# Kernel optimization log

Measured on AMD Instinct MI355X. Metric: run time of the kernel, lower is better.

## Reference

```python
import jax, jax.numpy as jnp
import numpy as np

NUM_HEADS = 12


def setup_inputs() -> dict:
    key = jax.random.key(0)
    k1, k2, k3 = jax.random.split(key, 3)
    B, N, C = 64, 320, 768
    x = jax.random.normal(k1, (B, N, C), dtype=jnp.float32)
    W_qkv = jax.random.normal(k2, (C, 3 * C), dtype=jnp.float32) * (C ** -0.5)
    W_proj = jax.random.normal(k3, (C, C), dtype=jnp.float32) * (C ** -0.5)
    b_proj = jnp.zeros((C,), dtype=jnp.float32)
    return {"x": x, "W_qkv": W_qkv, "W_proj": W_proj, "b_proj": b_proj,
            "t_h": 8, "t_w": 8, "s_h": 16, "s_w": 16}


def reference(x, W_qkv, W_proj, b_proj, t_h, t_w, s_h, s_w):
    B, N, C = x.shape
    H = NUM_HEADS
    Dh = C // H
    scale = Dh ** -0.5
    L = t_h * t_w  # template length; search length = s_h*s_w = N - L

    qkv = (x @ W_qkv).reshape(B, N, 3, H, Dh)
    q = jnp.transpose(qkv[:, :, 0], (0, 2, 1, 3))  # [B,H,N,Dh]
    k = jnp.transpose(qkv[:, :, 1], (0, 2, 1, 3))
    v = jnp.transpose(qkv[:, :, 2], (0, 2, 1, 3))

    q_mt, q_s = q[:, :, :L], q[:, :, L:]
    k_mt = k[:, :, :L]
    v_mt = v[:, :, :L]

    # Template self-attention (template attends only to template)
    attn_mt = jax.nn.softmax(jnp.einsum('bhqd,bhkd->bhqk', q_mt * scale, k_mt), axis=-1)
    x_mt = jnp.einsum('bhqk,bhkd->bhqd', attn_mt, v_mt)  # [B,H,L,Dh]

    # Search cross-attention (search attends to all tokens)
    attn_s = jax.nn.softmax(jnp.einsum('bhqd,bhkd->bhqk', q_s * scale, k), axis=-1)
    x_s = jnp.einsum('bhqk,bhkd->bhqd', attn_s, v)  # [B,H,N-L,Dh]

    x_mt = jnp.transpose(x_mt, (0, 2, 1, 3)).reshape(B, L, C)
    x_s = jnp.transpose(x_s, (0, 2, 1, 3)).reshape(B, N - L, C)
    out = jnp.concatenate([x_mt, x_s], axis=1)  # [B,N,C]
    out = out @ W_proj + b_proj
    return out
```

## Files before the change

### kernel.cpp

```cpp
#include <hip/hip_runtime.h>
#include <hip/hip_bf16.h>
#include <stdint.h>

#define BB 64
#define NN 320
#define CC 768
#define HH 12
#define DH 64
#define NC3 2304
#define MROWS (BB*NN)

typedef __attribute__((ext_vector_type(8))) short short8;
typedef __attribute__((ext_vector_type(4))) float f32x4;
typedef __attribute__((ext_vector_type(8))) __bf16 bf16x8;

union BF8U { short8 s; bf16x8 b; };
static __device__ __forceinline__ bf16x8 asbf(short8 v){ BF8U u; u.s = v; return u.b; }

#define MFMA16(a,b,c) __builtin_amdgcn_mfma_f32_16x16x32_bf16((a),(b),(c),0,0,0)

static __device__ __forceinline__ void gload16(const void* g, void* l){
  __builtin_amdgcn_global_load_lds(
      (const __attribute__((address_space(1))) void*)g,
      (__attribute__((address_space(3))) void*)l, 16, 0, 0);
}

__global__ __launch_bounds__(256) void convert_wT(
    const float* __restrict__ in, __hip_bfloat16* __restrict__ outT,
    int K, int Nc)
{
  __shared__ __hip_bfloat16 t[64][72];
  const int n0 = blockIdx.x * 64, k0 = blockIdx.y * 64;
  const int tid = threadIdx.x;
  const int tx = tid & 15, ty = tid >> 4;

  #pragma unroll
  for (int i = 0; i < 4; ++i){
    int kl = ty + i * 16;
    float4 v = *reinterpret_cast<const float4*>(&in[(size_t)(k0 + kl) * Nc + n0 + tx * 4]);
    t[tx*4+0][kl] = __float2bfloat16(v.x);
    t[tx*4+1][kl] = __float2bfloat16(v.y);
    t[tx*4+2][kl] = __float2bfloat16(v.z);
    t[tx*4+3][kl] = __float2bfloat16(v.w);
  }
  __syncthreads();
  #pragma unroll
  for (int j = 0; j < 2; ++j){
    int nl = (tid >> 3) + j * 32;
    int kl = (tid & 7) * 8;
    short8 v = *reinterpret_cast<const short8*>(&t[nl][kl]);
    *reinterpret_cast<short8*>(&outT[(size_t)(n0 + nl) * K + k0 + kl]) = v;
  }
}

__global__ __launch_bounds__(256) void convert_x(
    const float* __restrict__ X, __hip_bfloat16* __restrict__ Xb)
{
  size_t i = ((size_t)blockIdx.x * 256 + threadIdx.x) * 8;
  float4 a = *reinterpret_cast<const float4*>(&X[i]);
  float4 b = *reinterpret_cast<const float4*>(&X[i + 4]);
  __hip_bfloat16 t[8] = {__float2bfloat16(a.x), __float2bfloat16(a.y),
                         __float2bfloat16(a.z), __float2bfloat16(a.w),
                         __float2bfloat16(b.x), __float2bfloat16(b.y),
                         __float2bfloat16(b.z), __float2bfloat16(b.w)};
  *reinterpret_cast<short8*>(&Xb[i]) = *reinterpret_cast<const short8*>(t);
}

#define BM 128
#define BN 128
#define BK 64
#define NT (CC/BK)

__global__ __launch_bounds__(256, 4) void gemm_qkv(
    const __hip_bfloat16* __restrict__ Xb,
    const __hip_bfloat16* __restrict__ WT,
    __hip_bfloat16* __restrict__ qb,
    __hip_bfloat16* __restrict__ kb,
    __hip_bfloat16* __restrict__ vt)
{
  __shared__ __hip_bfloat16 As[BM][BK];
  __shared__ __hip_bfloat16 Bs[BN][BK];
  const int tid = threadIdx.x;
  const int bm = blockIdx.x * BM;
  const int bn = blockIdx.y * BN;
  const int w = tid >> 6, lane = tid & 63;
  const int wr = w >> 1, wc = w & 1;
  const int l16 = lane & 15, lq = lane >> 4;
  const int srow = lane >> 3;
  const int scol = ((lane & 7) ^ srow) * 8;
  const int rsw  = (l16 & 7) * 8;

  f32x4 acc[4][4];
  #pragma unroll
  for (int i = 0; i < 4; ++i)
    #pragma unroll
    for (int j = 0; j < 4; ++j) acc[i][j] = (f32x4){0.f,0.f,0.f,0.f};

  for (int k0 = 0; k0 < CC; k0 += BK){
    #pragma unroll
    for (int it = 0; it < 4; ++it){
      int c = w * 4 + it;
      int row = c * 8 + srow;
      gload16(&Xb[(size_t)(bm + row) * CC + k0 + scol], &As[0][0] + c * 512);
      gload16(&WT[(size_t)(bn + row) * CC + k0 + scol], &Bs[0][0] + c * 512);
    }
    __syncthreads();
    #pragma unroll
    for (int kc = 0; kc < 2; ++kc){
      const int acol = (kc*32 + lq*8) ^ rsw;
      short8 bfr[4];
      #pragma unroll
      for (int ni = 0; ni < 4; ++ni)
        bfr[ni] = *reinterpret_cast<const short8*>(&Bs[wc*64 + ni*16 + l16][acol]);
      #pragma unroll
      for (int mi = 0; mi < 4; ++mi){
        short8 af = *reinterpret_cast<const short8*>(&As[wr*64 + mi*16 + l16][acol]);
        #pragma unroll
        for (int ni = 0; ni < 4; ++ni)
          acc[mi][ni] = MFMA16(asbf(af), asbf(bfr[ni]), acc[mi][ni]);
      }
    }
    __syncthreads();
  }

  const int s = bn / CC;
  const int h = ((bn % CC) >> 6) + wc;
  if (s == 2){
    #pragma unroll
    for (int mi = 0; mi < 4; ++mi){
      const int rowbase = bm + wr*64 + mi*16 + lq*4;
      const int b  = rowbase / NN;
      const int n0 = rowbase - b * NN;
      const int bh = b * HH + h;
      #pragma unroll
      for (int ni = 0; ni < 4; ++ni){
        const int dh = ni*16 + l16;
        __hip_bfloat16 q4[4] = {__float2bfloat16(acc[mi][ni][0]),
                                __float2bfloat16(acc[mi][ni][1]),
                                __float2bfloat16(acc[mi][ni][2]),
                                __float2bfloat16(acc[mi][ni][3])};
        *reinterpret_cast<uint64_t*>(&vt[((size_t)bh * DH + dh) * NN + n0]) =
            *reinterpret_cast<const uint64_t*>(q4);
      }
    }
  } else {
    __hip_bfloat16* const dst = (s == 0) ? qb : kb;
    #pragma unroll
    for (int mi = 0; mi < 4; ++mi){
      const int rowbase = bm + wr*64 + mi*16 + lq*4;
      const int b  = rowbase / NN;
      const int n0 = rowbase - b * NN;
      const int bh = b * HH + h;
      #pragma unroll
      for (int r = 0; r < 4; ++r){
        __hip_bfloat16* rp = dst + ((size_t)bh * NN + n0 + r) * DH + l16;
        #pragma unroll
        for (int ni = 0; ni < 4; ++ni)
          rp[ni*16] = __float2bfloat16(acc[mi][ni][r]);
      }
    }
  }
}

template<int NKT>
__global__ __launch_bounds__(256) void attn_kernel(
    const __hip_bfloat16* __restrict__ qb,
    const __hip_bfloat16* __restrict__ kb,
    const __hip_bfloat16* __restrict__ vt,
    __hip_bfloat16* __restrict__ ob)
{
  constexpr int NTILE = NKT / 4;
  constexpr int NBUF  = (NTILE > 1) ? 2 : 1;
  __shared__ __hip_bfloat16 Kt[NBUF][64][64];
  __shared__ __hip_bfloat16 Vt[NBUF][64][64];
  __shared__ __hip_bfloat16 P[4][16][72];

  const int tid = threadIdx.x;
  const int w = tid >> 6, lane = tid & 63;
  const int l16 = lane & 15, lq = lane >> 4;
  const int srow = lane >> 3;
  const int scol = ((lane & 7) ^ srow) * 8;
  const int rsw  = (l16 & 7) * 8;

  int bh, qbase;
  if (NKT == 4){ bh = blockIdx.x;      qbase = 0; }
  else         { bh = blockIdx.x >> 2; qbase = 64 + (blockIdx.x & 3) * 64; }
  const int qrow0 = qbase + w * 16;

  const __hip_bfloat16* qp = qb + ((size_t)bh * NN + qrow0) * DH;
  const __hip_bfloat16* kp = kb + (size_t)bh * NN * DH;
  const __hip_bfloat16* vp = vt + (size_t)bh * DH * NN;

  short8 aq[2];
  #pragma unroll
  for (int kc = 0; kc < 2; ++kc)
    aq[kc] = *reinterpret_cast<const short8*>(&qp[l16 * DH + kc*32 + lq*8]);
  __builtin_amdgcn_sched_barrier(0);

  auto stageK = [&](int j){
    #pragma unroll
    for (int it = 0; it < 2; ++it){
      int c = w * 2 + it;
      gload16(&kp[(size_t)(j*64 + c*8 + srow) * DH + scol],
              &Kt[j & (NBUF-1)][0][0] + c * 512);
    }
  };
  auto stageV = [&](int j){
    #pragma unroll
    for (int it = 0; it < 2; ++it){
      int c = w * 2 + it;
      gload16(&vp[(size_t)(c*8 + srow) * NN + j*64 + scol],
              &Vt[j & (NBUF-1)][0][0] + c * 512);
    }
  };

  f32x4 s[NKT];
  #pragma unroll
  for (int kt = 0; kt < NKT; ++kt) s[kt] = (f32x4){0.f,0.f,0.f,0.f};

  stageK(0);
  if (NTILE > 1) stageK(1);
  #pragma unroll
  for (int j = 0; j < NTILE; ++j){
    if (j + 1 < NTILE) asm volatile("s_waitcnt vmcnt(2)" ::: "memory");
    else               asm volatile("s_waitcnt vmcnt(0)" ::: "memory");
    __builtin_amdgcn_s_barrier();
    #pragma unroll
    for (int kc = 0; kc < 2; ++kc){
      const int acol = (kc*32 + lq*8) ^ rsw;
      #pragma unroll
      for (int ktl = 0; ktl < 4; ++ktl){
        short8 bk = *reinterpret_cast<const short8*>(&Kt[j & (NBUF-1)][ktl*16 + l16][acol]);
        s[j*4 + ktl] = MFMA16(asbf(aq[kc]), asbf(bk), s[j*4 + ktl]);
      }
    }
    __builtin_amdgcn_s_barrier();
    if (j + 2 < NTILE) stageK(j + 2);
  }

  stageV(0);
  if (NTILE > 1) stageV(1);

  const float scale = 0.125f;
  float sum[4];
  #pragma unroll
  for (int r = 0; r < 4; ++r){
    float mx = -1e30f;
    #pragma unroll
    for (int kt = 0; kt < NKT; ++kt) mx = fmaxf(mx, s[kt][r]);
    #pragma unroll
    for (int off = 1; off < 16; off <<= 1) mx = fmaxf(mx, __shfl_xor(mx, off));
    float sm = 0.f;
    #pragma unroll
    for (int kt = 0; kt < NKT; ++kt){
      float p = __expf((s[kt][r] - mx) * scale);
      __hip_bfloat16 pb = __float2bfloat16(p);
      s[kt][r] = __bfloat162float(pb);
      sm += __bfloat162float(pb);
    }
    #pragma unroll
    for (int off = 1; off < 16; off <<= 1) sm += __shfl_xor(sm, off);
    sum[r] = sm;
  }

  f32x4 o[4];
  #pragma unroll
  for (int nt = 0; nt < 4; ++nt) o[nt] = (f32x4){0.f,0.f,0.f,0.f};
  #pragma unroll
  for (int j = 0; j < NTILE; ++j){
    if (j + 1 < NTILE) asm volatile("s_waitcnt vmcnt(2)" ::: "memory");
    else               asm volatile("s_waitcnt vmcnt(0)" ::: "memory");
    __builtin_amdgcn_s_barrier();
    #pragma unroll
    for (int ktl = 0; ktl < 4; ++ktl)
      #pragma unroll
      for (int r = 0; r < 4; ++r)
        P[w][lq*4 + r][ktl*16 + l16] = __float2bfloat16(s[j*4 + ktl][r]);
    #pragma unroll
    for (int kc = 0; kc < 2; ++kc){
      short8 ap = *reinterpret_cast<const short8*>(&P[w][l16][kc*32 + lq*8]);
      const int vcol = (kc*32 + lq*8) ^ rsw;
      #pragma unroll
      for (int nt = 0; nt < 4; ++nt){
        short8 bv = *reinterpret_cast<const short8*>(&Vt[j & (NBUF-1)][nt*16 + l16][vcol]);
        o[nt] = MFMA16(asbf(ap), asbf(bv), o[nt]);
      }
    }
    __builtin_amdgcn_s_barrier();
    if (j + 2 < NTILE) stageV(j + 2);
  }

  const int b = bh / HH, h = bh % HH;
  #pragma unroll
  for (int nt = 0; nt < 4; ++nt){
    #pragma unroll
    for (int r = 0; r < 4; ++r){
      int qrow = qrow0 + lq*4 + r;
      int dh = nt*16 + l16;
      float val = o[nt][r] / sum[r];
      ob[((size_t)b * NN + qrow) * CC + h * DH + dh] = __float2bfloat16(val);
    }
  }
}

__global__ __launch_bounds__(256, 4) void gemm_proj(
    const __hip_bfloat16* __restrict__ A,
    const __hip_bfloat16* __restrict__ WT,
    const float* __restrict__ bias,
    float* __restrict__ out)
{
  __shared__ __hip_bfloat16 As[BM][BK];
  __shared__ __hip_bfloat16 Bs[BN][BK];
  const int tid = threadIdx.x;
  const int bm = blockIdx.x * BM;
  const int bn = blockIdx.y * BN;
  const int w = tid >> 6, lane = tid & 63;
  const int wr = w >> 1, wc = w & 1;
  const int l16 = lane & 15, lq = lane >> 4;
  const int srow = lane >> 3;
  const int scol = ((lane & 7) ^ srow) * 8;
  const int rsw  = (l16 & 7) * 8;

  f32x4 acc[4][4];
  #pragma unroll
  for (int i = 0; i < 4; ++i)
    #pragma unroll
    for (int j = 0; j < 4; ++j) acc[i][j] = (f32x4){0.f,0.f,0.f,0.f};

  for (int k0 = 0; k0 < CC; k0 += BK){
    #pragma unroll
    for (int it = 0; it < 4; ++it){
      int c = w * 4 + it;
      int row = c * 8 + srow;
      gload16(&A [(size_t)(bm + row) * CC + k0 + scol], &As[0][0] + c * 512);
      gload16(&WT[(size_t)(bn + row) * CC + k0 + scol], &Bs[0][0] + c * 512);
    }
    __syncthreads();
    #pragma unroll
    for (int kc = 0; kc < 2; ++kc){
      const int acol = (kc*32 + lq*8) ^ rsw;
      short8 bfr[4];
      #pragma unroll
      for (int ni = 0; ni < 4; ++ni)
        bfr[ni] = *reinterpret_cast<const short8*>(&Bs[wc*64 + ni*16 + l16][acol]);
      #pragma unroll
      for (int mi = 0; mi < 4; ++mi){
        short8 af = *reinterpret_cast<const short8*>(&As[wr*64 + mi*16 + l16][acol]);
        #pragma unroll
        for (int ni = 0; ni < 4; ++ni)
          acc[mi][ni] = MFMA16(asbf(af), asbf(bfr[ni]), acc[mi][ni]);
      }
    }
    __syncthreads();
  }

  #pragma unroll
  for (int mi = 0; mi < 4; ++mi){
    #pragma unroll
    for (int ni = 0; ni < 4; ++ni){
      #pragma unroll
      for (int r = 0; r < 4; ++r){
        int row = bm + wr*64 + mi*16 + lq*4 + r;
        int col = bn + wc*64 + ni*16 + l16;
        out[(size_t)row * CC + col] = acc[mi][ni][r] + bias[col];
      }
    }
  }
}

extern "C" void kernel_launch(void* const* d_in, const int* in_sizes, int n_in,
                              void* d_out, int out_size, void* d_ws, size_t ws_size,
                              hipStream_t stream)
{
  const float* x     = (const float*)d_in[0];
  const float* Wqkv  = (const float*)d_in[1];
  const float* Wproj = (const float*)d_in[2];
  const float* bproj = (const float*)d_in[3];
  float* out = (float*)d_out;

  char* ws = (char*)d_ws;
  __hip_bfloat16* wqkvT  = (__hip_bfloat16*)ws; ws += (size_t)NC3 * CC * 2;
  __hip_bfloat16* wprojT = (__hip_bfloat16*)ws; ws += (size_t)CC * CC * 2;
  __hip_bfloat16* xb     = (__hip_bfloat16*)ws; ws += (size_t)MROWS * CC * 2;
  const size_t headsz = (size_t)BB * HH * NN * DH * 2;
  __hip_bfloat16* qb = (__hip_bfloat16*)ws; ws += headsz;
  __hip_bfloat16* kb = (__hip_bfloat16*)ws; ws += headsz;
  __hip_bfloat16* vt = (__hip_bfloat16*)ws; ws += headsz;
  __hip_bfloat16* ob = (__hip_bfloat16*)ws; ws += headsz;

  convert_wT<<<dim3(NC3/64, CC/64), 256, 0, stream>>>(Wqkv, wqkvT, CC, NC3);
  convert_wT<<<dim3(CC/64,  CC/64), 256, 0, stream>>>(Wproj, wprojT, CC, CC);
  convert_x<<<MROWS * CC / (256*8), 256, 0, stream>>>(x, xb);
  gemm_qkv<<<dim3(MROWS / BM, NC3 / BN), 256, 0, stream>>>(xb, wqkvT, qb, kb, vt);
  attn_kernel<4><<<BB * HH, 256, 0, stream>>>(qb, kb, vt, ob);
  attn_kernel<20><<<BB * HH * 4, 256, 0, stream>>>(qb, kb, vt, ob);
  gemm_proj<<<dim3(MROWS / BM, CC / BN), 256, 0, stream>>>(ob, wprojT, bproj, out);
}
```

Baseline: 205.1 us.

## Use online softmax in attention, fuse conversion kernels, raise attention occupancy

The attention kernel moves from a two-pass scheme (all scores held in registers, then softmax, then P·V) to a flash-style online softmax. Each K/V tile is loaded together, and the running max, sum and output are rescaled per tile. This is meant to cut register pressure (NKT=20 score vectors) so that launch_bounds(256,4) can give higher occupancy, and to overlap the K and V loads. The three fp32-to-bf16 conversion kernels are merged into one launch to save launch overhead. The cost is extra exponentials and rescaling per tile, plus more LDS traffic in flight.

```diff
diff --git a/kernel.cpp b/kernel.cpp
--- a/kernel.cpp
+++ b/kernel.cpp
@@ -25,15 +25,41 @@
       (__attribute__((address_space(3))) void*)l, 16, 0, 0);
 }
 
-__global__ __launch_bounds__(256) void convert_wT(
-    const float* __restrict__ in, __hip_bfloat16* __restrict__ outT,
-    int K, int Nc)
+#define XB  (MROWS*CC/2048)
+#define QTX (NC3/64)
+#define QTB (QTX*(CC/64))
+#define PTX (CC/64)
+#define PTB (PTX*(CC/64))
+
+__global__ __launch_bounds__(256) void convert_all(
+    const float* __restrict__ X, const float* __restrict__ Wqkv,
+    const float* __restrict__ Wproj,
+    __hip_bfloat16* __restrict__ Xb, __hip_bfloat16* __restrict__ wqkvT,
+    __hip_bfloat16* __restrict__ wprojT)
 {
   __shared__ __hip_bfloat16 t[64][72];
-  const int n0 = blockIdx.x * 64, k0 = blockIdx.y * 64;
+  int bid = blockIdx.x;
   const int tid = threadIdx.x;
+
+  if (bid < XB){
+    size_t i = ((size_t)bid * 256 + tid) * 8;
+    float4 a = *reinterpret_cast<const float4*>(&X[i]);
+    float4 b = *reinterpret_cast<const float4*>(&X[i + 4]);
+    __hip_bfloat16 tt[8] = {__float2bfloat16(a.x), __float2bfloat16(a.y),
+                            __float2bfloat16(a.z), __float2bfloat16(a.w),
+                            __float2bfloat16(b.x), __float2bfloat16(b.y),
+                            __float2bfloat16(b.z), __float2bfloat16(b.w)};
+    *reinterpret_cast<short8*>(&Xb[i]) = *reinterpret_cast<const short8*>(tt);
+    return;
+  }
+  bid -= XB;
+  const float* in; __hip_bfloat16* outT; int K, Nc, n0, k0;
+  if (bid < QTB){ in = Wqkv;  outT = wqkvT;  K = CC; Nc = NC3;
+                  n0 = (bid % QTX) * 64; k0 = (bid / QTX) * 64; }
+  else { bid -= QTB; in = Wproj; outT = wprojT; K = CC; Nc = CC;
+         n0 = (bid % PTX) * 64; k0 = (bid / PTX) * 64; }
+
   const int tx = tid & 15, ty = tid >> 4;
-
   #pragma unroll
   for (int i = 0; i < 4; ++i){
     int kl = ty + i * 16;
@@ -51,19 +77,6 @@
     short8 v = *reinterpret_cast<const short8*>(&t[nl][kl]);
     *reinterpret_cast<short8*>(&outT[(size_t)(n0 + nl) * K + k0 + kl]) = v;
   }
-}
-
-__global__ __launch_bounds__(256) void convert_x(
-    const float* __restrict__ X, __hip_bfloat16* __restrict__ Xb)
-{
-  size_t i = ((size_t)blockIdx.x * 256 + threadIdx.x) * 8;
-  float4 a = *reinterpret_cast<const float4*>(&X[i]);
-  float4 b = *reinterpret_cast<const float4*>(&X[i + 4]);
-  __hip_bfloat16 t[8] = {__float2bfloat16(a.x), __float2bfloat16(a.y),
-                         __float2bfloat16(a.z), __float2bfloat16(a.w),
-                         __float2bfloat16(b.x), __float2bfloat16(b.y),
-                         __float2bfloat16(b.z), __float2bfloat16(b.w)};
-  *reinterpret_cast<short8*>(&Xb[i]) = *reinterpret_cast<const short8*>(t);
 }
 
 #define BM 128
@@ -163,7 +176,7 @@
 }
 
 template<int NKT>
-__global__ __launch_bounds__(256) void attn_kernel(
+__global__ __launch_bounds__(256, 4) void attn_kernel(
     const __hip_bfloat16* __restrict__ qb,
     const __hip_bfloat16* __restrict__ kb,
     const __hip_bfloat16* __restrict__ vt,
@@ -214,68 +227,62 @@
     }
   };
 
-  f32x4 s[NKT];
-  #pragma unroll
-  for (int kt = 0; kt < NKT; ++kt) s[kt] = (f32x4){0.f,0.f,0.f,0.f};
-
-  stageK(0);
-  if (NTILE > 1) stageK(1);
+  float m[4] = {-1e30f, -1e30f, -1e30f, -1e30f};
+  float l[4] = {0.f, 0.f, 0.f, 0.f};
+  f32x4 o[4];
+  #pragma unroll
+  for (int nt = 0; nt < 4; ++nt) o[nt] = (f32x4){0.f,0.f,0.f,0.f};
+
+  const float scale = 0.125f;
+
+  stageK(0); stageV(0);
+  if (NTILE > 1){ stageK(1); stageV(1); }
+
   #pragma unroll
   for (int j = 0; j < NTILE; ++j){
-    if (j + 1 < NTILE) asm volatile("s_waitcnt vmcnt(2)" ::: "memory");
+    if (j + 1 < NTILE) asm volatile("s_waitcnt vmcnt(4)" ::: "memory");
     else               asm volatile("s_waitcnt vmcnt(0)" ::: "memory");
     __builtin_amdgcn_s_barrier();
+
+    f32x4 st[4];
+    #pragma unroll
+    for (int ktl = 0; ktl < 4; ++ktl) st[ktl] = (f32x4){0.f,0.f,0.f,0.f};
     #pragma unroll
     for (int kc = 0; kc < 2; ++kc){
       const int acol = (kc*32 + lq*8) ^ rsw;
       #pragma unroll
       for (int ktl = 0; ktl < 4; ++ktl){
         short8 bk = *reinterpret_cast<const short8*>(&Kt[j & (NBUF-1)][ktl*16 + l16][acol]);
-        s[j*4 + ktl] = MFMA16(asbf(aq[kc]), asbf(bk), s[j*4 + ktl]);
-      }
-    }
-    __builtin_amdgcn_s_barrier();
-    if (j + 2 < NTILE) stageK(j + 2);
-  }
-
-  stageV(0);
-  if (NTILE > 1) stageV(1);
-
-  const float scale = 0.125f;
-  float sum[4];
-  #pragma unroll
-  for (int r = 0; r < 4; ++r){
-    float mx = -1e30f;
-    #pragma unroll
-    for (int kt = 0; kt < NKT; ++kt) mx = fmaxf(mx, s[kt][r]);
-    #pragma unroll
-    for (int off = 1; off < 16; off <<= 1) mx = fmaxf(mx, __shfl_xor(mx, off));
-    float sm = 0.f;
-    #pragma unroll
-    for (int kt = 0; kt < NKT; ++kt){
-      float p = __expf((s[kt][r] - mx) * scale);
-      __hip_bfloat16 pb = __float2bfloat16(p);
-      s[kt][r] = __bfloat162float(pb);
-      sm += __bfloat162float(pb);
-    }
-    #pragma unroll
-    for (int off = 1; off < 16; off <<= 1) sm += __shfl_xor(sm, off);
-    sum[r] = sm;
-  }
-
-  f32x4 o[4];
-  #pragma unroll
-  for (int nt = 0; nt < 4; ++nt) o[nt] = (f32x4){0.f,0.f,0.f,0.f};
-  #pragma unroll
-  for (int j = 0; j < NTILE; ++j){
-    if (j + 1 < NTILE) asm volatile("s_waitcnt vmcnt(2)" ::: "memory");
-    else               asm volatile("s_waitcnt vmcnt(0)" ::: "memory");
-    __builtin_amdgcn_s_barrier();
-    #pragma unroll
-    for (int ktl = 0; ktl < 4; ++ktl)
-      #pragma unroll
-      for (int r = 0; r < 4; ++r)
-        P[w][lq*4 + r][ktl*16 + l16] = __float2bfloat16(s[j*4 + ktl][r]);
+        st[ktl] = MFMA16(asbf(aq[kc]), asbf(bk), st[ktl]);
+      }
+    }
+
+    float f[4];
+    #pragma unroll
+    for (int r = 0; r < 4; ++r){
+      float tmax = fmaxf(fmaxf(st[0][r], st[1][r]), fmaxf(st[2][r], st[3][r]));
+      #pragma unroll
+      for (int off = 1; off < 16; off <<= 1) tmax = fmaxf(tmax, __shfl_xor(tmax, off));
+      float mnew = fmaxf(m[r], tmax * scale);
+      f[r] = __expf(m[r] - mnew);
+      float sm = 0.f;
+      #pragma unroll
+      for (int ktl = 0; ktl < 4; ++ktl){
+        float p = __expf(st[ktl][r] * scale - mnew);
+        __hip_bfloat16 pb = __float2bfloat16(p);
+        P[w][lq*4 + r][ktl*16 + l16] = pb;
+        sm += __bfloat162float(pb);
+      }
+      #pragma unroll
+      for (int off = 1; off < 16; off <<= 1) sm += __shfl_xor(sm, off);
+      l[r] = l[r] * f[r] + sm;
+      m[r] = mnew;
+    }
+    #pragma unroll
+    for (int nt = 0; nt < 4; ++nt){
+      o[nt][0] *= f[0]; o[nt][1] *= f[1]; o[nt][2] *= f[2]; o[nt][3] *= f[3];
+    }
+
     #pragma unroll
     for (int kc = 0; kc < 2; ++kc){
       short8 ap = *reinterpret_cast<const short8*>(&P[w][l16][kc*32 + lq*8]);
@@ -286,8 +293,9 @@
         o[nt] = MFMA16(asbf(ap), asbf(bv), o[nt]);
       }
     }
+
     __builtin_amdgcn_s_barrier();
-    if (j + 2 < NTILE) stageV(j + 2);
+    if (j + 2 < NTILE){ stageK(j + 2); stageV(j + 2); }
   }
 
   const int b = bh / HH, h = bh % HH;
@@ -297,7 +305,7 @@
     for (int r = 0; r < 4; ++r){
       int qrow = qrow0 + lq*4 + r;
       int dh = nt*16 + l16;
-      float val = o[nt][r] / sum[r];
+      float val = o[nt][r] / l[r];
       ob[((size_t)b * NN + qrow) * CC + h * DH + dh] = __float2bfloat16(val);
     }
   }
@@ -388,9 +396,7 @@
   __hip_bfloat16* vt = (__hip_bfloat16*)ws; ws += headsz;
   __hip_bfloat16* ob = (__hip_bfloat16*)ws; ws += headsz;
 
-  convert_wT<<<dim3(NC3/64, CC/64), 256, 0, stream>>>(Wqkv, wqkvT, CC, NC3);
-  convert_wT<<<dim3(CC/64,  CC/64), 256, 0, stream>>>(Wproj, wprojT, CC, CC);
-  convert_x<<<MROWS * CC / (256*8), 256, 0, stream>>>(x, xb);
+  convert_all<<<XB + QTB + PTB, 256, 0, stream>>>(x, Wqkv, Wproj, xb, wqkvT, wprojT);
   gemm_qkv<<<dim3(MROWS / BM, NC3 / BN), 256, 0, stream>>>(xb, wqkvT, qb, kb, vt);
   attn_kernel<4><<<BB * HH, 256, 0, stream>>>(qb, kb, vt, ob);
   attn_kernel<20><<<BB * HH * 4, 256, 0, stream>>>(qb, kb, vt, ob);
```

After: 205.0 us. About the same (-0.0%).
